# Performance work log

Measured on AMD Instinct MI355X. Metric: run time of the kernel, lower is better.

## Reference

```python
import jax, jax.numpy as jnp
import numpy as np
from jax import lax

B, N, NUM_Q, H = 16, 64, 256, 64


def setup_inputs() -> dict:
    key = jax.random.key(0)
    ks = jax.random.split(key, 12)
    s = 0.05
    return {
        "q": jax.random.randint(ks[0], (B, N), 0, NUM_Q),
        "r": jax.random.randint(ks[1], (B, N), 0, 2),
        "x_emb": jax.random.normal(ks[2], (2 * NUM_Q, H), jnp.float32) * s,
        "q_emb": jax.random.normal(ks[3], (NUM_Q, H), jnp.float32) * s,
        "init_h": jax.random.normal(ks[4], (NUM_Q, H), jnp.float32) * s,
        "w1": jax.random.normal(ks[5], (2 * H, H), jnp.float32) * s,
        "b1": jnp.zeros((H,), jnp.float32),
        "w2": jax.random.normal(ks[6], (H, H), jnp.float32) * s,
        "b2": jnp.zeros((H,), jnp.float32),
        "w_ih": jax.random.normal(ks[7], (3 * H, 2 * H), jnp.float32) * s,
        "w_hh": jax.random.normal(ks[8], (3 * H, H), jnp.float32) * s,
        "b_ih": jnp.zeros((3 * H,), jnp.float32),
        "b_hh": jnp.zeros((3 * H,), jnp.float32),
        "bias": jnp.zeros((1, NUM_Q, 1), jnp.float32),
        "out_w": jax.random.normal(ks[9], (H,), jnp.float32) * s,
        "theta": jnp.asarray(0.0, jnp.float32),
    }


def reference(q, r, x_emb, q_emb, init_h, w1, b1, w2, b2, w_ih, w_hh, b_ih, b_hh, bias, out_w, theta):
    xe = x_emb[q + NUM_Q * r]                          # [B,N,H]
    mask = jax.nn.one_hot(q, NUM_Q, dtype=xe.dtype)    # [B,N,Q] one-hot of answered KC
    ht0 = jnp.broadcast_to(init_h, (B, NUM_Q, H))

    def gru_seq(x):
        # torch nn.GRU(batch_first=True) scanned over the num_q axis, h0 = 0.
        # x: [B,Q,2H] -> [B,Q,H]; gate order (r, z, n).
        gi = jnp.einsum('bqi,gi->bqg', x, w_ih) + b_ih  # [B,Q,3H]

        def cell(h, gi_t):
            gh = h @ w_hh.T + b_hh
            i_r, i_z, i_n = jnp.split(gi_t, 3, axis=-1)
            h_r, h_z, h_n = jnp.split(gh, 3, axis=-1)
            rg = jax.nn.sigmoid(i_r + h_r)
            zg = jax.nn.sigmoid(i_z + h_z)
            ng = jnp.tanh(i_n + rg * h_n)
            hn = (1.0 - zg) * ng + zg * h
            return hn, hn

        _, hs = lax.scan(cell, jnp.zeros((B, H), x.dtype), jnp.swapaxes(gi, 0, 1))
        return jnp.swapaxes(hs, 0, 1)

    def step(ht, inp):
        xe_t, m_t = inp                                  # [B,H], [B,Q]
        m3 = m_t[..., None]
        # aggregate: answered KC gets [h, x_emb], others get [h, q_emb]
        tail = m3 * xe_t[:, None, :] + (1.0 - m3) * q_emb[None]
        ht_cat = jnp.concatenate([ht, tail], axis=-1)    # [B,Q,2H]
        # f_self MLP (dropout = identity in eval); f_neighbor undefined in
        # source (pass) -> shared MLP stand-in, so m = mlp(ht_cat) everywhere.
        m = jnp.maximum(ht_cat @ w1 + b1, 0.0) @ w2 + b2
        ht_new = gru_seq(jnp.concatenate([m, ht], axis=-1))
        return ht_new, ht_new

    _, hs = lax.scan(step, ht0, (jnp.swapaxes(xe, 0, 1), jnp.swapaxes(mask, 0, 1)))
    h_full = jnp.concatenate([ht0[None], hs], axis=0).transpose(1, 0, 2, 3)  # [B,N+1,Q,H]

    # decayed-softmax attention over the growing history, vectorized over t.
    rate = jnp.exp(theta)
    sim = jnp.einsum('btd,cd->btc', q_emb[q], q_emb)     # [B,tau,Q]
    idx = jnp.arange(N)
    dt = idx[:, None] - idx[None, :]                     # t - tau, [N,N]
    decay = jnp.exp(-rate * jnp.maximum(dt, 0).astype(sim.dtype))
    neg = jnp.finfo(sim.dtype).min
    scores = jnp.where((dt >= 0)[None, :, :, None],
                       decay[None, :, :, None] * sim[:, None, :, :], neg)  # [B,t,tau,Q]
    alpha = jax.nn.softmax(scores, axis=2)               # softmax over history tau
    hread = jnp.einsum('btuc,bucf->btcf', alpha, h_full[:, :N])
    h_cur = h_full[:, 1:]                                # state after step t
    logits = jnp.einsum('btcf,f->btc', h_cur + hread, out_w) + bias.reshape(1, 1, NUM_Q)
    y = jax.nn.sigmoid(logits)                           # [B,N,Q]
    return y, h_full
```

## Files before the change

### kernel.cpp

```cpp
#include <hip/hip_runtime.h>
#include <math.h>

#define NB 16
#define NT 64
#define NQc 256
#define HD 64

#define WS_CB     0
#define WS_QE1    192
#define WS_XE1    16576
#define WS_G      82112
#define WS_HW     147648
#define WS_U16    413888
#define WS_WHH16  422080
#define WS_W2M16  428224
#define WS_I16    434368
#define WS_GFLAG  442560

typedef _Float16 h2 __attribute__((ext_vector_type(2)));

#if defined(__has_builtin)
#if __has_builtin(__builtin_amdgcn_fdot2)
#define FDOT2(a,b,c) __builtin_amdgcn_fdot2((a),(b),(c),false)
#endif
#endif
#ifndef FDOT2
__device__ inline float fdot2_sw(h2 a, h2 b, float c){ return c + (float)a[0]*(float)b[0] + (float)a[1]*(float)b[1]; }
#define FDOT2(a,b,c) fdot2_sw((a),(b),(c))
#endif

__device__ inline h2 H2(unsigned u){ union{unsigned x; h2 h;} v; v.x=u; return v.h; }
__device__ inline unsigned short F2H(float f){ union{_Float16 h; unsigned short s;} v; v.h=(_Float16)f; return v.s; }
__device__ inline unsigned PACK2(float a, float b){ return (unsigned)F2H(a) | ((unsigned)F2H(b)<<16); }

#define WGACQ(p)    __hip_atomic_load((p), __ATOMIC_ACQUIRE, __HIP_MEMORY_SCOPE_WORKGROUP)
#define WGREL(p,v)  __hip_atomic_store((p), (v), __ATOMIC_RELEASE, __HIP_MEMORY_SCOPE_WORKGROUP)
#define SPIN(p,tgt) while (WGACQ(p) < (tgt)) __builtin_amdgcn_s_sleep(1)

__global__ __launch_bounds__(256) void kPrep(
    const int* __restrict__ q, const int* __restrict__ r,
    const float* __restrict__ x_emb, const float* __restrict__ q_emb,
    const float* __restrict__ init_h, const float* __restrict__ w1,
    const float* __restrict__ b1, const float* __restrict__ w2,
    const float* __restrict__ b2, const float* __restrict__ w_ih,
    const float* __restrict__ w_hh, const float* __restrict__ b_ih,
    float* __restrict__ ws, float* __restrict__ h_full)
{
  int idx = blockIdx.x*256 + threadIdx.x;
  unsigned* wsu = (unsigned*)ws;
  if (idx < 192) {
    int g = idx; float s = b_ih[g];
    for (int j=0;j<64;j++) s += b2[j]*w_ih[g*128+j];
    ws[WS_CB+g] = s;
  } else if (idx < 16576) {
    int e = idx-192; int c = e>>6, i = e&63;
    float s = b1[i];
    for (int k=0;k<64;k++) s += q_emb[c*64+k]*w1[(64+k)*64+i];
    ws[WS_QE1+e] = s;
  } else if (idx < 82112) {
    int e = idx-16576; int bt = e>>6, i = e&63;
    int row = q[bt] + 256*r[bt];
    float s = b1[i];
    for (int k=0;k<64;k++) s += x_emb[row*64+k]*w1[(64+k)*64+i];
    ws[WS_XE1+e] = s;
  } else if (idx < 147648) {
    int e = idx-82112; int a = e>>8, cc = e&255;
    float s = 0.f;
    for (int d=0;d<64;d++) s += q_emb[a*64+d]*q_emb[cc*64+d];
    ws[WS_G+e] = s;
  } else if (idx < 409792) {
    int e = idx-147648; int bb = e>>14, cf = e&16383;
    h_full[(size_t)bb*65*16384 + cf] = init_h[cf];
  } else if (idx < 417984) {
    int e = idx-409792; int rr = e>>5, d = e&31;
    float v0, v1;
    if (rr < 64) { v0 = w1[(2*d)*64+rr];   v1 = w1[(2*d+1)*64+rr]; }
    else { int g = rr-64; v0 = w_ih[g*128+64+2*d]; v1 = w_ih[g*128+64+2*d+1]; }
    wsu[WS_U16+e] = PACK2(v0,v1);
  } else if (idx < 424128) {
    int e = idx-417984; int g = e>>5, d = e&31;
    wsu[WS_WHH16+e] = PACK2(w_hh[g*64+2*d], w_hh[g*64+2*d+1]);
  } else if (idx < 430272) {
    int e = idx-424128; int g = e>>5, d = e&31;
    float s0=0.f, s1=0.f;
    for (int j=0;j<64;j++){ float wij = w_ih[g*128+j]; s0 += w2[(2*d)*64+j]*wij; s1 += w2[(2*d+1)*64+j]*wij; }
    wsu[WS_W2M16+e] = PACK2(s0,s1);
  } else if (idx < 438464) {
    int e = idx-430272; int c = e>>5, d = e&31;
    wsu[WS_I16+e] = PACK2(init_h[c*64+2*d], init_h[c*64+2*d+1]);
  }
}

__global__ __launch_bounds__(512,2) void kA(
    const int* __restrict__ q, const float* __restrict__ b_hh,
    float* __restrict__ ws, float* __restrict__ h_full)
{
  __shared__ __align__(16) unsigned short h16s[4][16][64];
  __shared__ __align__(16) unsigned short inbox[16][64];
  __shared__ __align__(16) unsigned short a16s[4][8][64];
  __shared__ float h32s[4][8][64];
  __shared__ float gi3s[4][4][3][64];
  __shared__ int flgH[4], flgB[4], flgC[4];

  const int bid = blockIdx.x;
  const int b = bid & 15, tg = bid >> 4;
  const int tid = threadIdx.x, w = tid>>6, lane = tid&63;
  const bool isA = (w < 4);
  const int i = isA ? w : (w-4);
  const int t = tg*4 + i;

  const unsigned* U16  = (const unsigned*)ws + WS_U16;
  const unsigned* WH16 = (const unsigned*)ws + WS_WHH16;
  const unsigned* WM16 = (const unsigned*)ws + WS_W2M16;
  const unsigned* I16  = (const unsigned*)ws + WS_I16;
  const float* qe1 = ws + WS_QE1;
  const float* xe1 = ws + WS_XE1;
  const float* cb  = ws + WS_CB;
  unsigned* gflag  = (unsigned*)ws + WS_GFLAG;
  unsigned* hfu    = (unsigned*)h_full;

  if (tid < 4) { flgH[tid]=0; flgB[tid]=0; flgC[tid]=0; }
  if (isA) h16s[i][15][lane] = 0;
  __syncthreads();

  if (isA) {
    h2 wr[32], wz[32], wn[32], w2n[32];
    #pragma unroll
    for (int d=0; d<32; d++) {
      wr[d]  = H2(WH16[(lane)*32+d]);
      wz[d]  = H2(WH16[(64+lane)*32+d]);
      wn[d]  = H2(WH16[(128+lane)*32+d]);
      w2n[d] = H2(WM16[(128+lane)*32+d]);
    }
    const float bhr = b_hh[lane], bhz = b_hh[64+lane], bhn = b_hh[128+lane];
    float hreg = 0.f;

    SPIN(&flgB[i], 1);
    float gWn_cur = 0.f;
    {
      const uint4* ap = (const uint4*)a16s[i][0];
      #pragma unroll
      for (int k=0;k<8;k++){ uint4 c4 = ap[k];
        gWn_cur = FDOT2(w2n[4*k+0], H2(c4.x), gWn_cur);
        gWn_cur = FDOT2(w2n[4*k+1], H2(c4.y), gWn_cur);
        gWn_cur = FDOT2(w2n[4*k+2], H2(c4.z), gWn_cur);
        gWn_cur = FDOT2(w2n[4*k+3], H2(c4.w), gWn_cur);
      }
    }
    for (int c=0; c<256; c++) {
      int tgt = (c+2 <= 256) ? (c+2) : 256;
      SPIN(&flgB[i], tgt);
      float gWn_nxt = 0.f;
      if (c < 255) {
        const uint4* ap = (const uint4*)a16s[i][(c+1)&7];
        #pragma unroll
        for (int k=0;k<8;k++){ uint4 c4 = ap[k];
          gWn_nxt = FDOT2(w2n[4*k+0], H2(c4.x), gWn_nxt);
          gWn_nxt = FDOT2(w2n[4*k+1], H2(c4.y), gWn_nxt);
          gWn_nxt = FDOT2(w2n[4*k+2], H2(c4.z), gWn_nxt);
          gWn_nxt = FDOT2(w2n[4*k+3], H2(c4.w), gWn_nxt);
        }
      }
      float ghr = bhr, ghz = bhz, ghn = bhn;
      const uint4* hp = (const uint4*)h16s[i][(c+15)&15];
      #pragma unroll
      for (int k=0;k<8;k++){ uint4 c4 = hp[k];
        h2 p0=H2(c4.x), p1=H2(c4.y), p2=H2(c4.z), p3=H2(c4.w);
        ghr=FDOT2(wr[4*k+0],p0,ghr); ghr=FDOT2(wr[4*k+1],p1,ghr); ghr=FDOT2(wr[4*k+2],p2,ghr); ghr=FDOT2(wr[4*k+3],p3,ghr);
        ghz=FDOT2(wz[4*k+0],p0,ghz); ghz=FDOT2(wz[4*k+1],p1,ghz); ghz=FDOT2(wz[4*k+2],p2,ghz); ghz=FDOT2(wz[4*k+3],p3,ghz);
        ghn=FDOT2(wn[4*k+0],p0,ghn); ghn=FDOT2(wn[4*k+1],p1,ghn); ghn=FDOT2(wn[4*k+2],p2,ghn); ghn=FDOT2(wn[4*k+3],p3,ghn);
      }
      float gr  = gi3s[i][c&3][0][lane];
      float gzp = gi3s[i][c&3][1][lane];
      float gnp = gi3s[i][c&3][2][lane];
      float rg = 1.f/(1.f+__expf(-(gr+ghr)));
      float zg = 1.f/(1.f+__expf(-(gzp+ghz)));
      float xn = gnp + gWn_cur + rg*ghn;
      float e2 = __expf(2.f*xn);
      float ng = 1.f - 2.f/(e2+1.f);
      hreg = zg*hreg + (1.f-zg)*ng;
      if (i < 3) { SPIN(&flgB[i+1], c-15); }
      SPIN(&flgC[i], c-7);
      h16s[i][c&15][lane] = F2H(hreg);
      h32s[i][c&7][lane]  = hreg;
      if (lane == 0) WGREL(&flgH[i], c+1);
      gWn_cur = gWn_nxt;
    }
  } else {
    h2 u0[32],u1[32],u2[32],u3[32],m2r[32],m2z[32];
    #pragma unroll
    for (int d=0; d<32; d++) {
      u0[d] = H2(U16[(lane)*32+d]);
      u1[d] = H2(U16[(64+lane)*32+d]);
      u2[d] = H2(U16[(128+lane)*32+d]);
      u3[d] = H2(U16[(192+lane)*32+d]);
      m2r[d]= H2(WM16[(lane)*32+d]);
      m2z[d]= H2(WM16[(64+lane)*32+d]);
    }
    const float cbr = cb[lane], cbz = cb[64+lane], cbn = cb[128+lane];
    const int qrow = q[b*64+t];
    const float xr = xe1[(b*64+t)*64+lane];
    const unsigned* hfp = hfu + (size_t)(b*65 + 4*tg)*16384;
    unsigned* hfoU = hfu + (size_t)(b*65 + t + 1)*16384;
    float*    hfoF = h_full + (size_t)(b*65 + t + 1)*16384;
    unsigned* gfp = gflag + (b*16 + tg - 1);
    unsigned* gfc = gflag + (b*16 + tg);
    unsigned gv = 0;
    float e1cur = (qrow == 0) ? xr : qe1[lane];
    const unsigned short (*src)[64] = (i == 0) ? inbox : h16s[i-1];

    for (int s=0; s<256; s++) {
      SPIN(&flgH[i], s-3);
      if (i == 0) {
        unsigned short hv;
        if (tg == 0) {
          unsigned uu = I16[s*32 + (lane>>1)];
          hv = (lane&1) ? (unsigned short)(uu>>16) : (unsigned short)(uu&0xffff);
        } else {
          while (gv < (unsigned)(s+1)) {
            gv = __hip_atomic_load(gfp, __ATOMIC_RELAXED, __HIP_MEMORY_SCOPE_AGENT);
            if (gv < (unsigned)(s+1)) __builtin_amdgcn_s_sleep(2);
          }
          unsigned wv = __hip_atomic_load(&hfp[s*64+lane], __ATOMIC_RELAXED, __HIP_MEMORY_SCOPE_AGENT);
          union{unsigned u; float f;} cv; cv.u = wv;
          hv = F2H(cv.f);
        }
        inbox[s&15][lane] = hv;
        asm volatile("s_waitcnt lgkmcnt(0)" ::: "memory");
      } else {
        SPIN(&flgH[i-1], s+1);
      }
      float m1 = e1cur, gr = cbr, gz = cbz, gn = cbn;
      const uint4* rp = (const uint4*)src[s&15];
      #pragma unroll
      for (int k=0;k<8;k++){ uint4 c4 = rp[k];
        h2 p0=H2(c4.x), p1=H2(c4.y), p2=H2(c4.z), p3=H2(c4.w);
        m1=FDOT2(u0[4*k+0],p0,m1); m1=FDOT2(u0[4*k+1],p1,m1); m1=FDOT2(u0[4*k+2],p2,m1); m1=FDOT2(u0[4*k+3],p3,m1);
        gr=FDOT2(u1[4*k+0],p0,gr); gr=FDOT2(u1[4*k+1],p1,gr); gr=FDOT2(u1[4*k+2],p2,gr); gr=FDOT2(u1[4*k+3],p3,gr);
        gz=FDOT2(u2[4*k+0],p0,gz); gz=FDOT2(u2[4*k+1],p1,gz); gz=FDOT2(u2[4*k+2],p2,gz); gz=FDOT2(u2[4*k+3],p3,gz);
        gn=FDOT2(u3[4*k+0],p0,gn); gn=FDOT2(u3[4*k+1],p1,gn); gn=FDOT2(u3[4*k+2],p2,gn); gn=FDOT2(u3[4*k+3],p3,gn);
      }
      float av = fmaxf(m1, 0.f);
      a16s[i][s&7][lane] = F2H(av);
      asm volatile("s_waitcnt lgkmcnt(0)" ::: "memory");
      float g2r = 0.f, g2z = 0.f;
      {
        const uint4* ap = (const uint4*)a16s[i][s&7];
        #pragma unroll
        for (int k=0;k<8;k++){ uint4 c4 = ap[k];
          h2 p0=H2(c4.x), p1=H2(c4.y), p2=H2(c4.z), p3=H2(c4.w);
          g2r=FDOT2(m2r[4*k+0],p0,g2r); g2r=FDOT2(m2r[4*k+1],p1,g2r); g2r=FDOT2(m2r[4*k+2],p2,g2r); g2r=FDOT2(m2r[4*k+3],p3,g2r);
          g2z=FDOT2(m2z[4*k+0],p0,g2z); g2z=FDOT2(m2z[4*k+1],p1,g2z); g2z=FDOT2(m2z[4*k+2],p2,g2z); g2z=FDOT2(m2z[4*k+3],p3,g2z);
        }
      }
      gi3s[i][s&3][0][lane] = gr + g2r;
      gi3s[i][s&3][1][lane] = gz + g2z;
      gi3s[i][s&3][2][lane] = gn;
      if (lane == 0) WGREL(&flgB[i], s+1);
      if (s < 255) e1cur = ((s+1) == qrow) ? xr : qe1[(s+1)*64+lane];
      int cc = s-3;
      if (cc >= 0) {
        SPIN(&flgH[i], cc+1);
        float hv = h32s[i][cc&7][lane];
        if (i == 3) {
          union{float f; unsigned u;} cu; cu.f = hv;
          __hip_atomic_store(&hfoU[cc*64+lane], cu.u, __ATOMIC_RELAXED, __HIP_MEMORY_SCOPE_AGENT);
        } else {
          hfoF[cc*64+lane] = hv;
        }
        if (lane == 0) WGREL(&flgC[i], cc+1);
        if (i == 3 && (cc&3) == 3) {
          asm volatile("s_waitcnt vmcnt(0)" ::: "memory");
          if (lane == 0) __hip_atomic_store(gfc, (unsigned)(cc+1), __ATOMIC_RELAXED, __HIP_MEMORY_SCOPE_AGENT);
        }
      }
    }
    for (int cc=253; cc<256; cc++) {
      SPIN(&flgH[i], cc+1);
      float hv = h32s[i][cc&7][lane];
      if (i == 3) {
        union{float f; unsigned u;} cu; cu.f = hv;
        __hip_atomic_store(&hfoU[cc*64+lane], cu.u, __ATOMIC_RELAXED, __HIP_MEMORY_SCOPE_AGENT);
      } else {
        hfoF[cc*64+lane] = hv;
      }
      if (lane == 0) WGREL(&flgC[i], cc+1);
      if (i == 3 && (cc&3) == 3) {
        asm volatile("s_waitcnt vmcnt(0)" ::: "memory");
        if (lane == 0) __hip_atomic_store(gfc, (unsigned)(cc+1), __ATOMIC_RELAXED, __HIP_MEMORY_SCOPE_AGENT);
      }
    }
  }
}

__global__ __launch_bounds__(256) void kHw(const float* __restrict__ h_full,
    const float* __restrict__ out_w, float* __restrict__ hw)
{
  __shared__ float ow[64];
  if (threadIdx.x < 64) ow[threadIdx.x] = out_w[threadIdx.x];
  __syncthreads();
  const int blk = blockIdx.x, c = threadIdx.x;
  const float* hp = h_full + ((size_t)blk*256 + c)*64;
  float s = 0.f;
  #pragma unroll
  for (int f=0; f<64; f++) s += hp[f]*ow[f];
  hw[blk*256+c] = s;
}

__global__ __launch_bounds__(256) void kY(const int* __restrict__ q,
    const float* __restrict__ ws, const float* __restrict__ bias,
    const float* __restrict__ theta, float* __restrict__ y)
{
  const float* G  = ws + WS_G;
  const float* hw = ws + WS_HW;
  const int b = blockIdx.x >> 2, tq = blockIdx.x & 3;
  const int c = threadIdx.x;
  __shared__ float siml[64][256];
  for (int u=0; u<64; u++) {
    int qq = q[b*64+u];
    siml[u][c] = G[qq*256+c];
  }
  __syncthreads();
  const float rate = __expf(theta[0]);
  const float bv = bias[c];
  const float* hwb = hw + b*65*256;
  for (int tt=0; tt<16; tt++) {
    const int t = tq*16+tt;
    float mx = -1e30f;
    for (int u=0; u<=t; u++) {
      float s = __expf(-rate*(float)(t-u))*siml[u][c];
      mx = fmaxf(mx, s);
    }
    float se = 0.f, sw = 0.f;
    for (int u=0; u<=t; u++) {
      float s = __expf(-rate*(float)(t-u))*siml[u][c];
      float e = __expf(s-mx);
      se += e; sw += e*hwb[u*256+c];
    }
    float lg = hwb[(t+1)*256+c] + sw/se + bv;
    y[(b*64+t)*256+c] = 1.f/(1.f+__expf(-lg));
  }
}

extern "C" void kernel_launch(void* const* d_in, const int* in_sizes, int n_in,
                              void* d_out, int out_size, void* d_ws, size_t ws_size,
                              hipStream_t stream)
{
  (void)in_sizes; (void)n_in; (void)out_size; (void)ws_size;
  const int*   q      = (const int*)  d_in[0];
  const int*   r      = (const int*)  d_in[1];
  const float* x_emb  = (const float*)d_in[2];
  const float* q_emb  = (const float*)d_in[3];
  const float* init_h = (const float*)d_in[4];
  const float* w1     = (const float*)d_in[5];
  const float* b1     = (const float*)d_in[6];
  const float* w2     = (const float*)d_in[7];
  const float* b2     = (const float*)d_in[8];
  const float* w_ih   = (const float*)d_in[9];
  const float* w_hh   = (const float*)d_in[10];
  const float* b_ih   = (const float*)d_in[11];
  const float* b_hh   = (const float*)d_in[12];
  const float* bias   = (const float*)d_in[13];
  const float* out_w  = (const float*)d_in[14];
  const float* theta  = (const float*)d_in[15];

  float* out    = (float*)d_out;
  float* y      = out;
  float* h_full = out + 262144;
  float* ws     = (float*)d_ws;

  hipMemsetAsync((unsigned*)ws + WS_GFLAG, 0, 256*sizeof(unsigned), stream);
  kPrep<<<1713,256,0,stream>>>(q,r,x_emb,q_emb,init_h,w1,b1,w2,b2,w_ih,w_hh,b_ih,ws,h_full);
  {
    void* ka[] = { (void*)&q, (void*)&b_hh, (void*)&ws, (void*)&h_full };
    hipError_t e = hipLaunchCooperativeKernel((const void*)kA, dim3(256), dim3(512), ka, 0, stream);
    if (e != hipSuccess) {
      kA<<<dim3(256),dim3(512),0,stream>>>(q,b_hh,ws,h_full);
    }
  }
  kHw<<<1040,256,0,stream>>>(h_full, out_w, ws + WS_HW);
  kY<<<64,256,0,stream>>>(q, ws, bias, theta, y);
}
```

Before: 802.4 us.

## Rebalance GRU producer/consumer waves and prefetch inter-block h rows ahead

Moves the W2-derived r/z gate projections from the producer waves to the consumer (recurrent) waves, and moves the n-gate W2 term to the producer, which packs gate inputs into a float4 ring. The recurrent critical path no longer waits on separate flgB/flgC flags. The producer now prefetches upstream block rows four steps ahead from global memory instead of reading the init_h fp16 table, and the busy-wait sleep in the workgroup spin is removed. The aim is to shorten the serial per-step latency, at the cost of more register pressure on the recurrent wave and subtler flag ordering.

New measurement: 844.3 us. 5.2% more time.

```diff
diff --git a/kernel.cpp b/kernel.cpp
--- a/kernel.cpp
+++ b/kernel.cpp
@@ -1,10 +1,5 @@
 #include <hip/hip_runtime.h>
 #include <math.h>
-
-#define NB 16
-#define NT 64
-#define NQc 256
-#define HD 64
 
 #define WS_CB     0
 #define WS_QE1    192
@@ -33,9 +28,8 @@
 __device__ inline unsigned short F2H(float f){ union{_Float16 h; unsigned short s;} v; v.h=(_Float16)f; return v.s; }
 __device__ inline unsigned PACK2(float a, float b){ return (unsigned)F2H(a) | ((unsigned)F2H(b)<<16); }
 
-#define WGACQ(p)    __hip_atomic_load((p), __ATOMIC_ACQUIRE, __HIP_MEMORY_SCOPE_WORKGROUP)
+#define SPIN(p,tgt) while (__hip_atomic_load((p), __ATOMIC_ACQUIRE, __HIP_MEMORY_SCOPE_WORKGROUP) < (tgt)) {}
 #define WGREL(p,v)  __hip_atomic_store((p), (v), __ATOMIC_RELEASE, __HIP_MEMORY_SCOPE_WORKGROUP)
-#define SPIN(p,tgt) while (WGACQ(p) < (tgt)) __builtin_amdgcn_s_sleep(1)
 
 __global__ __launch_bounds__(256) void kPrep(
     const int* __restrict__ q, const int* __restrict__ r,
@@ -85,9 +79,6 @@
     float s0=0.f, s1=0.f;
     for (int j=0;j<64;j++){ float wij = w_ih[g*128+j]; s0 += w2[(2*d)*64+j]*wij; s1 += w2[(2*d+1)*64+j]*wij; }
     wsu[WS_W2M16+e] = PACK2(s0,s1);
-  } else if (idx < 438464) {
-    int e = idx-430272; int c = e>>5, d = e&31;
-    wsu[WS_I16+e] = PACK2(init_h[c*64+2*d], init_h[c*64+2*d+1]);
   }
 }
 
@@ -99,153 +90,48 @@
   __shared__ __align__(16) unsigned short inbox[16][64];
   __shared__ __align__(16) unsigned short a16s[4][8][64];
   __shared__ float h32s[4][8][64];
-  __shared__ float gi3s[4][4][3][64];
-  __shared__ int flgH[4], flgB[4], flgC[4];
-
-  const int bid = blockIdx.x;
-  const int b = bid & 15, tg = bid >> 4;
-  const int tid = threadIdx.x, w = tid>>6, lane = tid&63;
+  __shared__ __align__(16) float4 gi4s[4][4][64];
+  __shared__ int flgH[4], p2s[4];
+
+  const int bid = blockIdx.x, b = bid & 15, tg = bid >> 4;
+  const int tid = threadIdx.x, w = tid >> 6, lane = tid & 63;
   const bool isA = (w < 4);
-  const int i = isA ? w : (w-4);
+  const int i = isA ? w : (w - 4);
   const int t = tg*4 + i;
 
   const unsigned* U16  = (const unsigned*)ws + WS_U16;
   const unsigned* WH16 = (const unsigned*)ws + WS_WHH16;
   const unsigned* WM16 = (const unsigned*)ws + WS_W2M16;
-  const unsigned* I16  = (const unsigned*)ws + WS_I16;
   const float* qe1 = ws + WS_QE1;
   const float* xe1 = ws + WS_XE1;
   const float* cb  = ws + WS_CB;
-  unsigned* gflag  = (unsigned*)ws + WS_GFLAG;
-  unsigned* hfu    = (unsigned*)h_full;
-
-  if (tid < 4) { flgH[tid]=0; flgB[tid]=0; flgC[tid]=0; }
+  unsigned* gflag = (unsigned*)ws + WS_GFLAG;
+  unsigned* hfu = (unsigned*)h_full;
+
+  if (tid < 4) { flgH[tid] = 0; p2s[tid] = 0; }
   if (isA) h16s[i][15][lane] = 0;
   __syncthreads();
 
   if (isA) {
-    h2 wr[32], wz[32], wn[32], w2n[32];
+    h2 wr[32], wz[32], wn[32], m2r[32], m2z[32];
     #pragma unroll
     for (int d=0; d<32; d++) {
       wr[d]  = H2(WH16[(lane)*32+d]);
       wz[d]  = H2(WH16[(64+lane)*32+d]);
       wn[d]  = H2(WH16[(128+lane)*32+d]);
-      w2n[d] = H2(WM16[(128+lane)*32+d]);
+      m2r[d] = H2(WM16[(lane)*32+d]);
+      m2z[d] = H2(WM16[(64+lane)*32+d]);
     }
     const float bhr = b_hh[lane], bhz = b_hh[64+lane], bhn = b_hh[128+lane];
     float hreg = 0.f;
 
-    SPIN(&flgB[i], 1);
-    float gWn_cur = 0.f;
-    {
-      const uint4* ap = (const uint4*)a16s[i][0];
-      #pragma unroll
-      for (int k=0;k<8;k++){ uint4 c4 = ap[k];
-        gWn_cur = FDOT2(w2n[4*k+0], H2(c4.x), gWn_cur);
-        gWn_cur = FDOT2(w2n[4*k+1], H2(c4.y), gWn_cur);
-        gWn_cur = FDOT2(w2n[4*k+2], H2(c4.z), gWn_cur);
-        gWn_cur = FDOT2(w2n[4*k+3], H2(c4.w), gWn_cur);
-      }
-    }
     for (int c=0; c<256; c++) {
-      int tgt = (c+2 <= 256) ? (c+2) : 256;
-      SPIN(&flgB[i], tgt);
-      float gWn_nxt = 0.f;
-      if (c < 255) {
-        const uint4* ap = (const uint4*)a16s[i][(c+1)&7];
-        #pragma unroll
-        for (int k=0;k<8;k++){ uint4 c4 = ap[k];
-          gWn_nxt = FDOT2(w2n[4*k+0], H2(c4.x), gWn_nxt);
-          gWn_nxt = FDOT2(w2n[4*k+1], H2(c4.y), gWn_nxt);
-          gWn_nxt = FDOT2(w2n[4*k+2], H2(c4.z), gWn_nxt);
-          gWn_nxt = FDOT2(w2n[4*k+3], H2(c4.w), gWn_nxt);
-        }
-      }
-      float ghr = bhr, ghz = bhz, ghn = bhn;
-      const uint4* hp = (const uint4*)h16s[i][(c+15)&15];
-      #pragma unroll
-      for (int k=0;k<8;k++){ uint4 c4 = hp[k];
-        h2 p0=H2(c4.x), p1=H2(c4.y), p2=H2(c4.z), p3=H2(c4.w);
-        ghr=FDOT2(wr[4*k+0],p0,ghr); ghr=FDOT2(wr[4*k+1],p1,ghr); ghr=FDOT2(wr[4*k+2],p2,ghr); ghr=FDOT2(wr[4*k+3],p3,ghr);
-        ghz=FDOT2(wz[4*k+0],p0,ghz); ghz=FDOT2(wz[4*k+1],p1,ghz); ghz=FDOT2(wz[4*k+2],p2,ghz); ghz=FDOT2(wz[4*k+3],p3,ghz);
-        ghn=FDOT2(wn[4*k+0],p0,ghn); ghn=FDOT2(wn[4*k+1],p1,ghn); ghn=FDOT2(wn[4*k+2],p2,ghn); ghn=FDOT2(wn[4*k+3],p3,ghn);
-      }
-      float gr  = gi3s[i][c&3][0][lane];
-      float gzp = gi3s[i][c&3][1][lane];
-      float gnp = gi3s[i][c&3][2][lane];
-      float rg = 1.f/(1.f+__expf(-(gr+ghr)));
-      float zg = 1.f/(1.f+__expf(-(gzp+ghz)));
-      float xn = gnp + gWn_cur + rg*ghn;
-      float e2 = __expf(2.f*xn);
-      float ng = 1.f - 2.f/(e2+1.f);
-      hreg = zg*hreg + (1.f-zg)*ng;
-      if (i < 3) { SPIN(&flgB[i+1], c-15); }
-      SPIN(&flgC[i], c-7);
-      h16s[i][c&15][lane] = F2H(hreg);
-      h32s[i][c&7][lane]  = hreg;
-      if (lane == 0) WGREL(&flgH[i], c+1);
-      gWn_cur = gWn_nxt;
-    }
-  } else {
-    h2 u0[32],u1[32],u2[32],u3[32],m2r[32],m2z[32];
-    #pragma unroll
-    for (int d=0; d<32; d++) {
-      u0[d] = H2(U16[(lane)*32+d]);
-      u1[d] = H2(U16[(64+lane)*32+d]);
-      u2[d] = H2(U16[(128+lane)*32+d]);
-      u3[d] = H2(U16[(192+lane)*32+d]);
-      m2r[d]= H2(WM16[(lane)*32+d]);
-      m2z[d]= H2(WM16[(64+lane)*32+d]);
-    }
-    const float cbr = cb[lane], cbz = cb[64+lane], cbn = cb[128+lane];
-    const int qrow = q[b*64+t];
-    const float xr = xe1[(b*64+t)*64+lane];
-    const unsigned* hfp = hfu + (size_t)(b*65 + 4*tg)*16384;
-    unsigned* hfoU = hfu + (size_t)(b*65 + t + 1)*16384;
-    float*    hfoF = h_full + (size_t)(b*65 + t + 1)*16384;
-    unsigned* gfp = gflag + (b*16 + tg - 1);
-    unsigned* gfc = gflag + (b*16 + tg);
-    unsigned gv = 0;
-    float e1cur = (qrow == 0) ? xr : qe1[lane];
-    const unsigned short (*src)[64] = (i == 0) ? inbox : h16s[i-1];
-
-    for (int s=0; s<256; s++) {
-      SPIN(&flgH[i], s-3);
-      if (i == 0) {
-        unsigned short hv;
-        if (tg == 0) {
-          unsigned uu = I16[s*32 + (lane>>1)];
-          hv = (lane&1) ? (unsigned short)(uu>>16) : (unsigned short)(uu&0xffff);
-        } else {
-          while (gv < (unsigned)(s+1)) {
-            gv = __hip_atomic_load(gfp, __ATOMIC_RELAXED, __HIP_MEMORY_SCOPE_AGENT);
-            if (gv < (unsigned)(s+1)) __builtin_amdgcn_s_sleep(2);
-          }
-          unsigned wv = __hip_atomic_load(&hfp[s*64+lane], __ATOMIC_RELAXED, __HIP_MEMORY_SCOPE_AGENT);
-          union{unsigned u; float f;} cv; cv.u = wv;
-          hv = F2H(cv.f);
-        }
-        inbox[s&15][lane] = hv;
-        asm volatile("s_waitcnt lgkmcnt(0)" ::: "memory");
-      } else {
-        SPIN(&flgH[i-1], s+1);
-      }
-      float m1 = e1cur, gr = cbr, gz = cbz, gn = cbn;
-      const uint4* rp = (const uint4*)src[s&15];
-      #pragma unroll
-      for (int k=0;k<8;k++){ uint4 c4 = rp[k];
-        h2 p0=H2(c4.x), p1=H2(c4.y), p2=H2(c4.z), p3=H2(c4.w);
-        m1=FDOT2(u0[4*k+0],p0,m1); m1=FDOT2(u0[4*k+1],p1,m1); m1=FDOT2(u0[4*k+2],p2,m1); m1=FDOT2(u0[4*k+3],p3,m1);
-        gr=FDOT2(u1[4*k+0],p0,gr); gr=FDOT2(u1[4*k+1],p1,gr); gr=FDOT2(u1[4*k+2],p2,gr); gr=FDOT2(u1[4*k+3],p3,gr);
-        gz=FDOT2(u2[4*k+0],p0,gz); gz=FDOT2(u2[4*k+1],p1,gz); gz=FDOT2(u2[4*k+2],p2,gz); gz=FDOT2(u2[4*k+3],p3,gz);
-        gn=FDOT2(u3[4*k+0],p0,gn); gn=FDOT2(u3[4*k+1],p1,gn); gn=FDOT2(u3[4*k+2],p2,gn); gn=FDOT2(u3[4*k+3],p3,gn);
-      }
-      float av = fmaxf(m1, 0.f);
-      a16s[i][s&7][lane] = F2H(av);
-      asm volatile("s_waitcnt lgkmcnt(0)" ::: "memory");
+      if (((c&3)==0) && i<3) { SPIN(&p2s[i+1], c-12); }
+      SPIN(&p2s[i], c+1);
+      float4 gv = gi4s[i][c&3][lane];
       float g2r = 0.f, g2z = 0.f;
       {
-        const uint4* ap = (const uint4*)a16s[i][s&7];
+        const uint4* ap = (const uint4*)a16s[i][c&7];
         #pragma unroll
         for (int k=0;k<8;k++){ uint4 c4 = ap[k];
           h2 p0=H2(c4.x), p1=H2(c4.y), p2=H2(c4.z), p3=H2(c4.w);
@@ -253,42 +139,123 @@
           g2z=FDOT2(m2z[4*k+0],p0,g2z); g2z=FDOT2(m2z[4*k+1],p1,g2z); g2z=FDOT2(m2z[4*k+2],p2,g2z); g2z=FDOT2(m2z[4*k+3],p3,g2z);
         }
       }
-      gi3s[i][s&3][0][lane] = gr + g2r;
-      gi3s[i][s&3][1][lane] = gz + g2z;
-      gi3s[i][s&3][2][lane] = gn;
-      if (lane == 0) WGREL(&flgB[i], s+1);
-      if (s < 255) e1cur = ((s+1) == qrow) ? xr : qe1[(s+1)*64+lane];
-      int cc = s-3;
-      if (cc >= 0) {
-        SPIN(&flgH[i], cc+1);
-        float hv = h32s[i][cc&7][lane];
+      float ghr = bhr, ghz = bhz, ghn = bhn;
+      {
+        const uint4* hp = (const uint4*)h16s[i][(c+15)&15];
+        #pragma unroll
+        for (int k=0;k<8;k++){ uint4 c4 = hp[k];
+          h2 p0=H2(c4.x), p1=H2(c4.y), p2=H2(c4.z), p3=H2(c4.w);
+          ghr=FDOT2(wr[4*k+0],p0,ghr); ghr=FDOT2(wr[4*k+1],p1,ghr); ghr=FDOT2(wr[4*k+2],p2,ghr); ghr=FDOT2(wr[4*k+3],p3,ghr);
+          ghz=FDOT2(wz[4*k+0],p0,ghz); ghz=FDOT2(wz[4*k+1],p1,ghz); ghz=FDOT2(wz[4*k+2],p2,ghz); ghz=FDOT2(wz[4*k+3],p3,ghz);
+          ghn=FDOT2(wn[4*k+0],p0,ghn); ghn=FDOT2(wn[4*k+1],p1,ghn); ghn=FDOT2(wn[4*k+2],p2,ghn); ghn=FDOT2(wn[4*k+3],p3,ghn);
+        }
+      }
+      float rg = 1.f/(1.f+__expf(-(gv.x + g2r + ghr)));
+      float zg = 1.f/(1.f+__expf(-(gv.y + g2z + ghz)));
+      float xn = gv.z + rg*ghn;
+      float e2 = __expf(2.f*xn);
+      float ng = 1.f - 2.f/(e2+1.f);
+      hreg = zg*hreg + (1.f-zg)*ng;
+      h16s[i][c&15][lane] = F2H(hreg);
+      h32s[i][c&7][lane]  = hreg;
+      if (lane == 0) WGREL(&flgH[i], c+1);
+    }
+  } else {
+    h2 u0[32],u1[32],u2[32],u3[32],w2n[32];
+    #pragma unroll
+    for (int d=0; d<32; d++) {
+      u0[d]  = H2(U16[(lane)*32+d]);
+      u1[d]  = H2(U16[(64+lane)*32+d]);
+      u2[d]  = H2(U16[(128+lane)*32+d]);
+      u3[d]  = H2(U16[(192+lane)*32+d]);
+      w2n[d] = H2(WM16[(128+lane)*32+d]);
+    }
+    const float cbr = cb[lane], cbz = cb[64+lane], cbn = cb[128+lane];
+    const int qrow = q[b*64+t];
+    const float xr = xe1[(b*64+t)*64+lane];
+    const unsigned* hfp = hfu + (size_t)(b*65 + 4*tg)*16384;
+    float*    hfoF = h_full + (size_t)(b*65 + t + 1)*16384;
+    unsigned* hfoU = hfu + (size_t)(b*65 + t + 1)*16384;
+    unsigned* gfp = gflag + (b*16 + tg - 1);
+    unsigned* gfc = gflag + (b*16 + tg);
+    const bool needFlag = (i==3) && (tg < 15);
+    unsigned gv = 0;
+
+    if (i == 0) {
+      if (tg > 0) {
+        while ((gv = __hip_atomic_load(gfp, __ATOMIC_RELAXED, __HIP_MEMORY_SCOPE_AGENT)) < 4u)
+          __builtin_amdgcn_s_sleep(1);
+      }
+      for (int rr=0; rr<4; rr++) {
+        union{unsigned u; float f;} cv;
+        cv.u = __hip_atomic_load(&hfp[rr*64+lane], __ATOMIC_RELAXED, __HIP_MEMORY_SCOPE_AGENT);
+        inbox[rr][lane] = F2H(cv.f);
+      }
+    }
+    float e1cur = (qrow == 0) ? xr : qe1[lane];
+    float prP=0.f, pzP=0.f, pnP=0.f;
+
+    for (int s=0; s<=260; s++) {
+      int tgt = s-4; if (tgt > 256) tgt = 256;
+      SPIN(&flgH[i], tgt);
+      float vrow = 0.f;
+      const bool havePf = (i==0) && (s+4 <= 255);
+      if (havePf) {
+        if (tg > 0) {
+          while (gv < (unsigned)(s+5)) {
+            gv = __hip_atomic_load(gfp, __ATOMIC_RELAXED, __HIP_MEMORY_SCOPE_AGENT);
+            if (gv < (unsigned)(s+5)) __builtin_amdgcn_s_sleep(1);
+          }
+        }
+        union{unsigned u; float f;} cv;
+        cv.u = __hip_atomic_load(&hfp[(s+4)*64+lane], __ATOMIC_RELAXED, __HIP_MEMORY_SCOPE_AGENT);
+        vrow = cv.f;
+      }
+      float pr=0.f, pz=0.f, pn=0.f;
+      if (s <= 255) {
+        if (i > 0) { SPIN(&flgH[i-1], s+1); }
+        const uint4* rp = (const uint4*)((i==0) ? inbox[s&15] : h16s[i-1][s&15]);
+        float m1 = e1cur; pr = cbr; pz = cbz; pn = cbn;
+        #pragma unroll
+        for (int k=0;k<8;k++){ uint4 c4 = rp[k];
+          h2 p0=H2(c4.x), p1=H2(c4.y), p2=H2(c4.z), p3=H2(c4.w);
+          m1=FDOT2(u0[4*k+0],p0,m1); m1=FDOT2(u0[4*k+1],p1,m1); m1=FDOT2(u0[4*k+2],p2,m1); m1=FDOT2(u0[4*k+3],p3,m1);
+          pr=FDOT2(u1[4*k+0],p0,pr); pr=FDOT2(u1[4*k+1],p1,pr); pr=FDOT2(u1[4*k+2],p2,pr); pr=FDOT2(u1[4*k+3],p3,pr);
+          pz=FDOT2(u2[4*k+0],p0,pz); pz=FDOT2(u2[4*k+1],p1,pz); pz=FDOT2(u2[4*k+2],p2,pz); pz=FDOT2(u2[4*k+3],p3,pz);
+          pn=FDOT2(u3[4*k+0],p0,pn); pn=FDOT2(u3[4*k+1],p1,pn); pn=FDOT2(u3[4*k+2],p2,pn); pn=FDOT2(u3[4*k+3],p3,pn);
+        }
+        float av = fmaxf(m1, 0.f);
+        a16s[i][s&7][lane] = F2H(av);
+      }
+      if (s >= 1 && s <= 256) {
+        int sm = s-1;
+        float g2n = 0.f;
+        const uint4* ap = (const uint4*)a16s[i][sm&7];
+        #pragma unroll
+        for (int k=0;k<8;k++){ uint4 c4 = ap[k];
+          g2n=FDOT2(w2n[4*k+0],H2(c4.x),g2n); g2n=FDOT2(w2n[4*k+1],H2(c4.y),g2n);
+          g2n=FDOT2(w2n[4*k+2],H2(c4.z),g2n); g2n=FDOT2(w2n[4*k+3],H2(c4.w),g2n);
+        }
+        gi4s[i][sm&3][lane] = make_float4(prP, pzP, pnP + g2n, 0.f);
+      }
+      if (s <= 255) { prP = pr; pzP = pz; pnP = pn; }
+      int r = s-5;
+      if (r >= 0) {
+        float hv = h32s[i][r&7][lane];
         if (i == 3) {
           union{float f; unsigned u;} cu; cu.f = hv;
-          __hip_atomic_store(&hfoU[cc*64+lane], cu.u, __ATOMIC_RELAXED, __HIP_MEMORY_SCOPE_AGENT);
+          __hip_atomic_store(&hfoU[r*64+lane], cu.u, __ATOMIC_RELAXED, __HIP_MEMORY_SCOPE_AGENT);
         } else {
-          hfoF[cc*64+lane] = hv;
-        }
-        if (lane == 0) WGREL(&flgC[i], cc+1);
-        if (i == 3 && (cc&3) == 3) {
+          hfoF[r*64+lane] = hv;
+        }
+        if (needFlag && ((r&3)==3)) {
           asm volatile("s_waitcnt vmcnt(0)" ::: "memory");
-          if (lane == 0) __hip_atomic_store(gfc, (unsigned)(cc+1), __ATOMIC_RELAXED, __HIP_MEMORY_SCOPE_AGENT);
-        }
-      }
-    }
-    for (int cc=253; cc<256; cc++) {
-      SPIN(&flgH[i], cc+1);
-      float hv = h32s[i][cc&7][lane];
-      if (i == 3) {
-        union{float f; unsigned u;} cu; cu.f = hv;
-        __hip_atomic_store(&hfoU[cc*64+lane], cu.u, __ATOMIC_RELAXED, __HIP_MEMORY_SCOPE_AGENT);
-      } else {
-        hfoF[cc*64+lane] = hv;
-      }
-      if (lane == 0) WGREL(&flgC[i], cc+1);
-      if (i == 3 && (cc&3) == 3) {
-        asm volatile("s_waitcnt vmcnt(0)" ::: "memory");
-        if (lane == 0) __hip_atomic_store(gfc, (unsigned)(cc+1), __ATOMIC_RELAXED, __HIP_MEMORY_SCOPE_AGENT);
-      }
+          if (lane == 0) __hip_atomic_store(gfc, (unsigned)(r+1), __ATOMIC_RELAXED, __HIP_MEMORY_SCOPE_AGENT);
+        }
+      }
+      if (havePf) inbox[(s+4)&15][lane] = F2H(vrow);
+      if (lane == 0) WGREL(&p2s[i], s);
+      if (s < 255) e1cur = ((s+1) == qrow) ? xr : qe1[(s+1)*64+lane];
     }
   }
 }
@@ -370,7 +337,7 @@
   float* ws     = (float*)d_ws;
 
   hipMemsetAsync((unsigned*)ws + WS_GFLAG, 0, 256*sizeof(unsigned), stream);
-  kPrep<<<1713,256,0,stream>>>(q,r,x_emb,q_emb,init_h,w1,b1,w2,b2,w_ih,w_hh,b_ih,ws,h_full);
+  kPrep<<<1681,256,0,stream>>>(q,r,x_emb,q_emb,init_h,w1,b1,w2,b2,w_ih,w_hh,b_ih,ws,h_full);
   {
     void* ka[] = { (void*)&q, (void*)&b_hh, (void*)&ws, (void*)&h_full };
     hipError_t e = hipLaunchCooperativeKernel((const void*)kA, dim3(256), dim3(512), ka, 0, stream);
```
